# Performance work log

Measured on AMD Instinct MI355X. Metric: run time of the kernel, lower is better.

## Reference

```python
import jax, jax.numpy as jnp
import numpy as np

DIM = 192
WH, WW = 8, 8
N = WH * WW
NUM_HEADS = 6
HEAD_DIM = DIM // NUM_HEADS
SCALE = HEAD_DIM ** (-0.5)
B_ = 4096


def _relative_position_index(Wh, Ww):
    coords = np.stack(np.meshgrid(np.arange(Wh), np.arange(Ww), indexing='ij'))  # [2, Wh, Ww]
    cf = coords.reshape(2, -1)                              # [2, N]
    rel = cf[:, :, None] - cf[:, None, :]                   # [2, N, N]
    rel = rel.transpose(1, 2, 0).astype(np.int64)           # [N, N, 2]
    rel[..., 0] += Wh - 1
    rel[..., 1] += Ww - 1
    rel[..., 0] *= 2 * Ww - 1
    return rel.sum(-1)                                      # [N, N]


REL_IDX = jnp.asarray(_relative_position_index(WH, WW))


def setup_inputs() -> dict:
    key = jax.random.key(0)
    ks = jax.random.split(key, 6)
    x = jax.random.normal(ks[0], (B_, N, DIM), dtype=jnp.float32)
    w_qkv = jax.random.normal(ks[1], (3 * DIM, DIM), dtype=jnp.float32) * (DIM ** -0.5)
    b_qkv = jnp.zeros((3 * DIM,), dtype=jnp.float32)
    w_proj = jax.random.normal(ks[2], (DIM, DIM), dtype=jnp.float32) * (DIM ** -0.5)
    b_proj = jnp.zeros((DIM,), dtype=jnp.float32)
    # torch init is zeros; use small noise so the bias path is exercised
    bias_table = jax.random.normal(ks[3], ((2 * WH - 1) * (2 * WW - 1), NUM_HEADS), dtype=jnp.float32) * 0.02
    return {"x": x, "w_qkv": w_qkv, "b_qkv": b_qkv, "w_proj": w_proj,
            "b_proj": b_proj, "bias_table": bias_table}


def reference(x, w_qkv, b_qkv, w_proj, b_proj, bias_table):
    B, n, C = x.shape
    qkv = jnp.einsum('bnc,dc->bnd', x, w_qkv) + b_qkv        # [B, N, 3C]
    qkv = qkv.reshape(B, n, 3, NUM_HEADS, HEAD_DIM)
    q = qkv[:, :, 0].transpose(0, 2, 1, 3) * SCALE            # [B, H, N, hd]
    k = qkv[:, :, 1].transpose(0, 2, 1, 3)
    v = qkv[:, :, 2].transpose(0, 2, 1, 3)
    attn = jnp.einsum('bhnd,bhmd->bhnm', q, k)                # [B, H, N, N]
    bias = bias_table[REL_IDX]                                # [N, N, H]
    attn = attn + bias.transpose(2, 0, 1)[None]               # broadcast over B
    attn = jax.nn.softmax(attn, axis=-1)
    out = jnp.einsum('bhnm,bhmd->bnhd', attn, v).reshape(B, n, C)
    return jnp.einsum('bnc,dc->bnd', out, w_proj) + b_proj
```

## Files before the change

kernel.cpp:

```cpp
#include <hip/hip_runtime.h>

#define TOK 64
#define CDIM 192
#define NH 6
#define HD 32
#define THREADS 384
#define QSCALE 0.17677669529663687f

#define WQ16_OFF 0
#define WP16_OFF 110592
#define BIAS_OFF 147456
#define WS_HALFS (147456 + 24576)
#define WS_BYTES (WS_HALFS * 2)

typedef _Float16 f16x8 __attribute__((ext_vector_type(8)));
typedef _Float16 f16x4 __attribute__((ext_vector_type(4)));
typedef float f32x4 __attribute__((ext_vector_type(4)));

__device__ __forceinline__ f16x8 ld8(const _Float16* p) {
  return *reinterpret_cast<const f16x8*>(p);
}

__device__ __forceinline__ f16x8 cvt8(const float* __restrict__ p) {
  float4 a = *reinterpret_cast<const float4*>(p);
  float4 c = *reinterpret_cast<const float4*>(p + 4);
  f16x8 r;
  r[0] = (_Float16)a.x; r[1] = (_Float16)a.y; r[2] = (_Float16)a.z; r[3] = (_Float16)a.w;
  r[4] = (_Float16)c.x; r[5] = (_Float16)c.y; r[6] = (_Float16)c.z; r[7] = (_Float16)c.w;
  return r;
}

__device__ __forceinline__ f16x4 pack4(float a, float b, float c, float d) {
  f16x4 r;
  r[0] = (_Float16)a; r[1] = (_Float16)b; r[2] = (_Float16)c; r[3] = (_Float16)d;
  return r;
}

__global__ void prep_ws(const float* __restrict__ wq, const float* __restrict__ wp,
                        const float* __restrict__ bt, _Float16* __restrict__ ws) {
  int i = blockIdx.x * 256 + threadIdx.x;
  if (i < 27648) {
    float4 v = reinterpret_cast<const float4*>(wq)[i];
    f16x4 h;
    h[0] = (_Float16)v.x; h[1] = (_Float16)v.y; h[2] = (_Float16)v.z; h[3] = (_Float16)v.w;
    *reinterpret_cast<f16x4*>(ws + WQ16_OFF + (size_t)i * 4) = h;
  } else if (i < 36864) {
    int j = i - 27648;
    float4 v = reinterpret_cast<const float4*>(wp)[j];
    f16x4 h;
    h[0] = (_Float16)v.x; h[1] = (_Float16)v.y; h[2] = (_Float16)v.z; h[3] = (_Float16)v.w;
    *reinterpret_cast<f16x4*>(ws + WP16_OFF + (size_t)j * 4) = h;
  } else if (i < 61440) {
    int j = i - 36864;
    int hit = j >> 10;
    int l = (j >> 4) & 63;
    int s = j & 15;
    int h = hit >> 2, it = hit & 3;
    int ii = it * 16 + (l & 15);
    int jj = (s >> 2) * 16 + (l >> 4) * 4 + (s & 3);
    int rel = ((ii >> 3) - (jj >> 3) + 7) * 15 + ((ii & 7) - (jj & 7) + 7);
    ws[BIAS_OFF + j] = (_Float16)bt[rel * NH + h];
  }
}

template <bool WS>
__global__ __launch_bounds__(THREADS, 4) void winattn(
    const float* __restrict__ x, const float* __restrict__ w_qkv,
    const float* __restrict__ b_qkv, const float* __restrict__ w_proj,
    const float* __restrict__ b_proj, const float* __restrict__ bias_table,
    const _Float16* __restrict__ ws, float* __restrict__ out) {
  __shared__ __align__(16) _Float16 R1[12288];

  const int tid = threadIdx.x;
  const int h   = tid >> 6;
  const int l   = tid & 63;
  const int l15 = l & 15;
  const int lg  = l >> 4;
  const int b   = blockIdx.x;
  const int sA0 = l15 ^ lg;
  const int sA1 = sA0 ^ 4;
  const f32x4 vzero = {0.f, 0.f, 0.f, 0.f};

  const float* xg = x + (size_t)b * (TOK * CDIM);
#pragma unroll
  for (int kk = 0; kk < 4; ++kk) {
    int q = tid + kk * THREADS;
    int n = q / 24;
    int p = q - n * 24;
    const float* src = xg + q * 8;
    float4 v0 = *reinterpret_cast<const float4*>(src);
    float4 v1 = *reinterpret_cast<const float4*>(src + 4);
    f16x8 h8;
    h8[0] = (_Float16)v0.x; h8[1] = (_Float16)v0.y;
    h8[2] = (_Float16)v0.z; h8[3] = (_Float16)v0.w;
    h8[4] = (_Float16)v1.x; h8[5] = (_Float16)v1.y;
    h8[6] = (_Float16)v1.z; h8[7] = (_Float16)v1.w;
    *reinterpret_cast<f16x8*>(&R1[(p * TOK + (n ^ (p & 7))) * 8]) = h8;
  }
  __syncthreads();

  const _Float16* bxb0 = &R1[(lg * TOK + sA0) * 8];
  const _Float16* bxb1 = &R1[(lg * TOK + sA1) * 8];

  f32x4 aq[2][4], ak[2][4];
#pragma unroll
  for (int mt = 0; mt < 2; ++mt)
#pragma unroll
    for (int nt = 0; nt < 4; ++nt) { aq[mt][nt] = vzero; ak[mt][nt] = vzero; }
  {
    const _Float16* pq0;
    const _Float16* pq1;
    const _Float16* pk0;
    const _Float16* pk1;
    const float* fq0; const float* fq1; const float* fk0; const float* fk1;
    if constexpr (WS) {
      pq0 = ws + WQ16_OFF + (size_t)(h * HD + l15) * CDIM + lg * 8;
      pq1 = pq0 + (size_t)16 * CDIM;
      pk0 = pq0 + (size_t)CDIM * CDIM;
      pk1 = pk0 + (size_t)16 * CDIM;
    } else {
      fq0 = w_qkv + (size_t)(h * HD + l15) * CDIM + lg * 8;
      fq1 = fq0 + (size_t)16 * CDIM;
      fk0 = fq0 + (size_t)CDIM * CDIM;
      fk1 = fk0 + (size_t)16 * CDIM;
    }
#pragma unroll
    for (int ks = 0; ks < 6; ++ks) {
      const _Float16* bb = (ks & 1) ? bxb1 : bxb0;
      f16x8 bx[4];
#pragma unroll
      for (int nt = 0; nt < 4; ++nt)
        bx[nt] = ld8(bb + ks * 2048 + nt * 128);
      f16x8 wqa[2], wka[2];
      if constexpr (WS) {
        wqa[0] = ld8(pq0 + ks * 32); wqa[1] = ld8(pq1 + ks * 32);
        wka[0] = ld8(pk0 + ks * 32); wka[1] = ld8(pk1 + ks * 32);
      } else {
        wqa[0] = cvt8(fq0 + ks * 32); wqa[1] = cvt8(fq1 + ks * 32);
        wka[0] = cvt8(fk0 + ks * 32); wka[1] = cvt8(fk1 + ks * 32);
      }
      __builtin_amdgcn_s_setprio(1);
#pragma unroll
      for (int mt = 0; mt < 2; ++mt)
#pragma unroll
        for (int nt = 0; nt < 4; ++nt) {
          aq[mt][nt] = __builtin_amdgcn_mfma_f32_16x16x32_f16(wqa[mt], bx[nt], aq[mt][nt], 0, 0, 0);
          ak[mt][nt] = __builtin_amdgcn_mfma_f32_16x16x32_f16(wka[mt], bx[nt], ak[mt][nt], 0, 0, 0);
        }
      __builtin_amdgcn_s_setprio(0);
    }
  }
  f16x4 qp[2][4], kp[2][4];
#pragma unroll
  for (int mt = 0; mt < 2; ++mt) {
    float4 bq = *reinterpret_cast<const float4*>(b_qkv + h * HD + mt * 16 + lg * 4);
    float4 bk = *reinterpret_cast<const float4*>(b_qkv + CDIM + h * HD + mt * 16 + lg * 4);
#pragma unroll
    for (int nt = 0; nt < 4; ++nt) {
      qp[mt][nt] = pack4((aq[mt][nt][0] + bq.x) * QSCALE, (aq[mt][nt][1] + bq.y) * QSCALE,
                         (aq[mt][nt][2] + bq.z) * QSCALE, (aq[mt][nt][3] + bq.w) * QSCALE);
      kp[mt][nt] = pack4(ak[mt][nt][0] + bk.x, ak[mt][nt][1] + bk.y,
                         ak[mt][nt][2] + bk.z, ak[mt][nt][3] + bk.w);
    }
  }

  f16x4 vp[4][2];
  {
    f32x4 av[4][2];
#pragma unroll
    for (int mt = 0; mt < 4; ++mt)
#pragma unroll
      for (int ct = 0; ct < 2; ++ct) av[mt][ct] = vzero;
    const _Float16* pv0;
    const _Float16* pv1;
    const float* fv0; const float* fv1;
    if constexpr (WS) {
      pv0 = ws + WQ16_OFF + (size_t)(2 * CDIM + h * HD + l15) * CDIM + lg * 8;
      pv1 = pv0 + (size_t)16 * CDIM;
    } else {
      fv0 = w_qkv + (size_t)(2 * CDIM + h * HD + l15) * CDIM + lg * 8;
      fv1 = fv0 + (size_t)16 * CDIM;
    }
#pragma unroll
    for (int ks = 0; ks < 6; ++ks) {
      const _Float16* bb = (ks & 1) ? bxb1 : bxb0;
      f16x8 a[4];
#pragma unroll
      for (int mt = 0; mt < 4; ++mt)
        a[mt] = ld8(bb + ks * 2048 + mt * 128);
      f16x8 bw[2];
      if constexpr (WS) { bw[0] = ld8(pv0 + ks * 32); bw[1] = ld8(pv1 + ks * 32); }
      else              { bw[0] = cvt8(fv0 + ks * 32); bw[1] = cvt8(fv1 + ks * 32); }
      __builtin_amdgcn_s_setprio(1);
#pragma unroll
      for (int mt = 0; mt < 4; ++mt)
#pragma unroll
        for (int ct = 0; ct < 2; ++ct)
          av[mt][ct] = __builtin_amdgcn_mfma_f32_16x16x32_f16(a[mt], bw[ct], av[mt][ct], 0, 0, 0);
      __builtin_amdgcn_s_setprio(0);
    }
    float bv0 = b_qkv[2 * CDIM + h * HD + l15];
    float bv1 = b_qkv[2 * CDIM + h * HD + 16 + l15];
#pragma unroll
    for (int s = 0; s < 4; ++s) {
      vp[s][0] = pack4(av[s][0][0] + bv0, av[s][0][1] + bv0, av[s][0][2] + bv0, av[s][0][3] + bv0);
      vp[s][1] = pack4(av[s][1][0] + bv1, av[s][1][1] + bv1, av[s][1][2] + bv1, av[s][1][3] + bv1);
    }
  }
  __syncthreads();

#pragma unroll
  for (int it = 0; it < 4; ++it) {
    f32x4 st[4];
    __builtin_amdgcn_s_setprio(1);
#pragma unroll
    for (int jt = 0; jt < 4; ++jt) {
      st[jt] = __builtin_amdgcn_mfma_f32_16x16x16f16(kp[0][jt], qp[0][it], vzero, 0, 0, 0);
      st[jt] = __builtin_amdgcn_mfma_f32_16x16x16f16(kp[1][jt], qp[1][it], st[jt], 0, 0, 0);
    }
    __builtin_amdgcn_s_setprio(0);
    if constexpr (WS) {
      const _Float16* bw = ws + BIAS_OFF + ((h * 4 + it) * 64 + l) * 16;
      f16x8 b0 = ld8(bw), b1 = ld8(bw + 8);
#pragma unroll
      for (int jt = 0; jt < 4; ++jt)
#pragma unroll
        for (int r = 0; r < 4; ++r)
          st[jt][r] += (float)((jt < 2) ? b0[jt * 4 + r] : b1[(jt - 2) * 4 + r]);
    } else {
      int i = it * 16 + l15, yi = i >> 3, xi = i & 7;
#pragma unroll
      for (int jt = 0; jt < 4; ++jt)
#pragma unroll
        for (int r = 0; r < 4; ++r) {
          int j = jt * 16 + lg * 4 + r, yj = j >> 3, xj = j & 7;
          st[jt][r] += bias_table[(((yi - yj + 7) * 15 + (xi - xj + 7)) * NH + h)];
        }
    }
    float m = st[0][0];
#pragma unroll
    for (int jt = 0; jt < 4; ++jt)
#pragma unroll
      for (int r = 0; r < 4; ++r) m = fmaxf(m, st[jt][r]);
    m = fmaxf(m, __shfl_xor(m, 16, 64));
    m = fmaxf(m, __shfl_xor(m, 32, 64));
    float sum = 0.f;
#pragma unroll
    for (int jt = 0; jt < 4; ++jt)
#pragma unroll
      for (int r = 0; r < 4; ++r) { st[jt][r] = __expf(st[jt][r] - m); sum += st[jt][r]; }
    sum += __shfl_xor(sum, 16, 64);
    sum += __shfl_xor(sum, 32, 64);
    float inv = 1.f / sum;
    f32x4 o[2] = {vzero, vzero};
#pragma unroll
    for (int s = 0; s < 4; ++s) {
      f16x4 pp = pack4(st[s][0] * inv, st[s][1] * inv, st[s][2] * inv, st[s][3] * inv);
      __builtin_amdgcn_s_setprio(1);
      o[0] = __builtin_amdgcn_mfma_f32_16x16x16f16(pp, vp[s][0], o[0], 0, 0, 0);
      o[1] = __builtin_amdgcn_mfma_f32_16x16x16f16(pp, vp[s][1], o[1], 0, 0, 0);
      __builtin_amdgcn_s_setprio(0);
    }
#pragma unroll
    for (int ct = 0; ct < 2; ++ct) {
      int c = h * HD + ct * 16 + l15;
      int op = c >> 3, s7 = op & 7;
      int lgx = lg ^ (s7 >> 2);
      int base = (op * TOK + it * 16 + lgx * 4) * 8 + (c & 7);
#pragma unroll
      for (int r = 0; r < 4; ++r)
        R1[base + (r ^ (s7 & 3)) * 8] = (_Float16)o[ct][r];
    }
  }
  __syncthreads();

  {
    const int e0 = h * 16 + l15;
    const int e1 = e0 + 96;
    f32x4 pa0[4], pa1[4];
#pragma unroll
    for (int mt = 0; mt < 4; ++mt) { pa0[mt] = vzero; pa1[mt] = vzero; }
    const _Float16* pw0;
    const _Float16* pw1;
    const float* fw0; const float* fw1;
    if constexpr (WS) {
      pw0 = ws + WP16_OFF + (size_t)e0 * CDIM + lg * 8;
      pw1 = pw0 + (size_t)96 * CDIM;
    } else {
      fw0 = w_proj + (size_t)e0 * CDIM + lg * 8;
      fw1 = fw0 + (size_t)96 * CDIM;
    }
#pragma unroll
    for (int ks = 0; ks < 6; ++ks) {
      const _Float16* bb = (ks & 1) ? bxb1 : bxb0;
      f16x8 a[4];
#pragma unroll
      for (int mt = 0; mt < 4; ++mt)
        a[mt] = ld8(bb + ks * 2048 + mt * 128);
      f16x8 w0, w1;
      if constexpr (WS) { w0 = ld8(pw0 + ks * 32); w1 = ld8(pw1 + ks * 32); }
      else              { w0 = cvt8(fw0 + ks * 32); w1 = cvt8(fw1 + ks * 32); }
      __builtin_amdgcn_s_setprio(1);
#pragma unroll
      for (int mt = 0; mt < 4; ++mt) {
        pa0[mt] = __builtin_amdgcn_mfma_f32_16x16x32_f16(a[mt], w0, pa0[mt], 0, 0, 0);
        pa1[mt] = __builtin_amdgcn_mfma_f32_16x16x32_f16(a[mt], w1, pa1[mt], 0, 0, 0);
      }
      __builtin_amdgcn_s_setprio(0);
    }
    float bp0 = b_proj[e0], bp1 = b_proj[e1];
#pragma unroll
    for (int mt = 0; mt < 4; ++mt) {
#pragma unroll
      for (int r = 0; r < 4; ++r) {
        int n = mt * 16 + lg * 4 + r;
        out[((size_t)b * TOK + n) * CDIM + e0] = pa0[mt][r] + bp0;
        out[((size_t)b * TOK + n) * CDIM + e1] = pa1[mt][r] + bp1;
      }
    }
  }
}

extern "C" void kernel_launch(void* const* d_in, const int* in_sizes, int n_in,
                              void* d_out, int out_size, void* d_ws, size_t ws_size,
                              hipStream_t stream) {
  const float* x          = (const float*)d_in[0];
  const float* w_qkv      = (const float*)d_in[1];
  const float* b_qkv      = (const float*)d_in[2];
  const float* w_proj     = (const float*)d_in[3];
  const float* b_proj     = (const float*)d_in[4];
  const float* bias_table = (const float*)d_in[5];
  float* out = (float*)d_out;
  int B = in_sizes[0] / (TOK * CDIM);

  if (ws_size >= (size_t)WS_BYTES) {
    _Float16* ws = (_Float16*)d_ws;
    hipLaunchKernelGGL(prep_ws, dim3(240), dim3(256), 0, stream,
                       w_qkv, w_proj, bias_table, ws);
    hipLaunchKernelGGL(winattn<true>, dim3(B), dim3(THREADS), 0, stream,
                       x, w_qkv, b_qkv, w_proj, b_proj, bias_table, ws, out);
  } else {
    hipLaunchKernelGGL(winattn<false>, dim3(B), dim3(THREADS), 0, stream,
                       x, w_qkv, b_qkv, w_proj, b_proj, bias_table,
                       (const _Float16*)nullptr, out);
  }
}
```

Measured before the change: 242.8 us.

## Make window attention persistent with double-buffered x prefetch

Converts the one-block-per-window kernel into a persistent kernel capped at 512 blocks. Each block loops over windows and prefetches the next window's x into registers during the output projection, then stores it into a second LDS buffer. The projection MFMA operands are swapped so each lane writes float4 rows of output instead of scalar stores. This costs double the LDS (48KB per block), which may limit occupancy, and leaves fewer blocks in flight to hide latency.

```diff
diff --git a/kernel.cpp b/kernel.cpp
--- a/kernel.cpp
+++ b/kernel.cpp
@@ -5,6 +5,7 @@
 #define NH 6
 #define HD 32
 #define THREADS 384
+#define GRID_MAX 512
 #define QSCALE 0.17677669529663687f
 
 #define WQ16_OFF 0
@@ -24,6 +25,13 @@
 __device__ __forceinline__ f16x8 cvt8(const float* __restrict__ p) {
   float4 a = *reinterpret_cast<const float4*>(p);
   float4 c = *reinterpret_cast<const float4*>(p + 4);
+  f16x8 r;
+  r[0] = (_Float16)a.x; r[1] = (_Float16)a.y; r[2] = (_Float16)a.z; r[3] = (_Float16)a.w;
+  r[4] = (_Float16)c.x; r[5] = (_Float16)c.y; r[6] = (_Float16)c.z; r[7] = (_Float16)c.w;
+  return r;
+}
+
+__device__ __forceinline__ f16x8 cvt2(float4 a, float4 c) {
   f16x8 r;
   r[0] = (_Float16)a.x; r[1] = (_Float16)a.y; r[2] = (_Float16)a.z; r[3] = (_Float16)a.w;
   r[4] = (_Float16)c.x; r[5] = (_Float16)c.y; r[6] = (_Float16)c.z; r[7] = (_Float16)c.w;
@@ -68,62 +76,79 @@
     const float* __restrict__ x, const float* __restrict__ w_qkv,
     const float* __restrict__ b_qkv, const float* __restrict__ w_proj,
     const float* __restrict__ b_proj, const float* __restrict__ bias_table,
-    const _Float16* __restrict__ ws, float* __restrict__ out) {
-  __shared__ __align__(16) _Float16 R1[12288];
+    const _Float16* __restrict__ ws, float* __restrict__ out, int B) {
+  __shared__ __align__(16) _Float16 X[2][12288];
 
   const int tid = threadIdx.x;
   const int h   = tid >> 6;
   const int l   = tid & 63;
   const int l15 = l & 15;
   const int lg  = l >> 4;
-  const int b   = blockIdx.x;
   const int sA0 = l15 ^ lg;
   const int sA1 = sA0 ^ 4;
+  const int G   = gridDim.x;
   const f32x4 vzero = {0.f, 0.f, 0.f, 0.f};
 
-  const float* xg = x + (size_t)b * (TOK * CDIM);
+  int goff[4], soff[4];
 #pragma unroll
   for (int kk = 0; kk < 4; ++kk) {
     int q = tid + kk * THREADS;
     int n = q / 24;
-    int p = q - n * 24;
-    const float* src = xg + q * 8;
-    float4 v0 = *reinterpret_cast<const float4*>(src);
-    float4 v1 = *reinterpret_cast<const float4*>(src + 4);
-    f16x8 h8;
-    h8[0] = (_Float16)v0.x; h8[1] = (_Float16)v0.y;
-    h8[2] = (_Float16)v0.z; h8[3] = (_Float16)v0.w;
-    h8[4] = (_Float16)v1.x; h8[5] = (_Float16)v1.y;
-    h8[6] = (_Float16)v1.z; h8[7] = (_Float16)v1.w;
-    *reinterpret_cast<f16x8*>(&R1[(p * TOK + (n ^ (p & 7))) * 8]) = h8;
+    int pp = q - n * 24;
+    goff[kk] = q * 8;
+    soff[kk] = (pp * TOK + (n ^ (pp & 7))) * 8;
+  }
+
+  const _Float16 *pq0 = nullptr, *pq1 = nullptr, *pk0 = nullptr, *pk1 = nullptr,
+                 *pv0 = nullptr, *pv1 = nullptr, *pw0 = nullptr, *pw1 = nullptr;
+  const float *fq0 = nullptr, *fq1 = nullptr, *fk0 = nullptr, *fk1 = nullptr,
+              *fv0 = nullptr, *fv1 = nullptr, *fw0 = nullptr, *fw1 = nullptr;
+  if constexpr (WS) {
+    pq0 = ws + WQ16_OFF + (size_t)(h * HD + l15) * CDIM + lg * 8;
+    pq1 = pq0 + (size_t)16 * CDIM;
+    pk0 = pq0 + (size_t)CDIM * CDIM;
+    pk1 = pk0 + (size_t)16 * CDIM;
+    pv0 = pq0 + (size_t)2 * CDIM * CDIM;
+    pv1 = pv0 + (size_t)16 * CDIM;
+    pw0 = ws + WP16_OFF + (size_t)(h * 16 + l15) * CDIM + lg * 8;
+    pw1 = pw0 + (size_t)96 * CDIM;
+  } else {
+    fq0 = w_qkv + (size_t)(h * HD + l15) * CDIM + lg * 8;
+    fq1 = fq0 + (size_t)16 * CDIM;
+    fk0 = fq0 + (size_t)CDIM * CDIM;
+    fk1 = fk0 + (size_t)16 * CDIM;
+    fv0 = fq0 + (size_t)2 * CDIM * CDIM;
+    fv1 = fv0 + (size_t)16 * CDIM;
+    fw0 = w_proj + (size_t)(h * 16 + l15) * CDIM + lg * 8;
+    fw1 = fw0 + (size_t)96 * CDIM;
+  }
+
+  {
+    const float* xg = x + (size_t)blockIdx.x * (TOK * CDIM);
+#pragma unroll
+    for (int kk = 0; kk < 4; ++kk) {
+      float4 v0 = *reinterpret_cast<const float4*>(xg + goff[kk]);
+      float4 v1 = *reinterpret_cast<const float4*>(xg + goff[kk] + 4);
+      *reinterpret_cast<f16x8*>(&X[0][soff[kk]]) = cvt2(v0, v1);
+    }
   }
   __syncthreads();
 
-  const _Float16* bxb0 = &R1[(lg * TOK + sA0) * 8];
-  const _Float16* bxb1 = &R1[(lg * TOK + sA1) * 8];
-
-  f32x4 aq[2][4], ak[2][4];
-#pragma unroll
-  for (int mt = 0; mt < 2; ++mt)
-#pragma unroll
-    for (int nt = 0; nt < 4; ++nt) { aq[mt][nt] = vzero; ak[mt][nt] = vzero; }
-  {
-    const _Float16* pq0;
-    const _Float16* pq1;
-    const _Float16* pk0;
-    const _Float16* pk1;
-    const float* fq0; const float* fq1; const float* fk0; const float* fk1;
-    if constexpr (WS) {
-      pq0 = ws + WQ16_OFF + (size_t)(h * HD + l15) * CDIM + lg * 8;
-      pq1 = pq0 + (size_t)16 * CDIM;
-      pk0 = pq0 + (size_t)CDIM * CDIM;
-      pk1 = pk0 + (size_t)16 * CDIM;
-    } else {
-      fq0 = w_qkv + (size_t)(h * HD + l15) * CDIM + lg * 8;
-      fq1 = fq0 + (size_t)16 * CDIM;
-      fk0 = fq0 + (size_t)CDIM * CDIM;
-      fk1 = fk0 + (size_t)16 * CDIM;
-    }
+  int p = 0;
+  const int NW = (B + G - 1) / G;
+#pragma unroll 1
+  for (int wi = 0; wi < NW; ++wi) {
+    const int win = blockIdx.x + wi * G;
+    if (win >= B) break;
+    _Float16* Xa = X[p];
+    const _Float16* bxb0 = &Xa[(lg * TOK + sA0) * 8];
+    const _Float16* bxb1 = &Xa[(lg * TOK + sA1) * 8];
+
+    f32x4 aq[2][4], ak[2][4];
+#pragma unroll
+    for (int mt = 0; mt < 2; ++mt)
+#pragma unroll
+      for (int nt = 0; nt < 4; ++nt) { aq[mt][nt] = vzero; ak[mt][nt] = vzero; }
 #pragma unroll
     for (int ks = 0; ks < 6; ++ks) {
       const _Float16* bb = (ks & 1) ? bxb1 : bxb0;
@@ -149,175 +174,181 @@
         }
       __builtin_amdgcn_s_setprio(0);
     }
-  }
-  f16x4 qp[2][4], kp[2][4];
-#pragma unroll
-  for (int mt = 0; mt < 2; ++mt) {
-    float4 bq = *reinterpret_cast<const float4*>(b_qkv + h * HD + mt * 16 + lg * 4);
-    float4 bk = *reinterpret_cast<const float4*>(b_qkv + CDIM + h * HD + mt * 16 + lg * 4);
-#pragma unroll
-    for (int nt = 0; nt < 4; ++nt) {
-      qp[mt][nt] = pack4((aq[mt][nt][0] + bq.x) * QSCALE, (aq[mt][nt][1] + bq.y) * QSCALE,
-                         (aq[mt][nt][2] + bq.z) * QSCALE, (aq[mt][nt][3] + bq.w) * QSCALE);
-      kp[mt][nt] = pack4(ak[mt][nt][0] + bk.x, ak[mt][nt][1] + bk.y,
-                         ak[mt][nt][2] + bk.z, ak[mt][nt][3] + bk.w);
-    }
-  }
-
-  f16x4 vp[4][2];
-  {
-    f32x4 av[4][2];
-#pragma unroll
-    for (int mt = 0; mt < 4; ++mt)
-#pragma unroll
-      for (int ct = 0; ct < 2; ++ct) av[mt][ct] = vzero;
-    const _Float16* pv0;
-    const _Float16* pv1;
-    const float* fv0; const float* fv1;
-    if constexpr (WS) {
-      pv0 = ws + WQ16_OFF + (size_t)(2 * CDIM + h * HD + l15) * CDIM + lg * 8;
-      pv1 = pv0 + (size_t)16 * CDIM;
-    } else {
-      fv0 = w_qkv + (size_t)(2 * CDIM + h * HD + l15) * CDIM + lg * 8;
-      fv1 = fv0 + (size_t)16 * CDIM;
-    }
-#pragma unroll
-    for (int ks = 0; ks < 6; ++ks) {
-      const _Float16* bb = (ks & 1) ? bxb1 : bxb0;
-      f16x8 a[4];
+    f16x4 qp[2][4], kp[2][4];
+#pragma unroll
+    for (int mt = 0; mt < 2; ++mt) {
+      float4 bq = *reinterpret_cast<const float4*>(b_qkv + h * HD + mt * 16 + lg * 4);
+      float4 bk = *reinterpret_cast<const float4*>(b_qkv + CDIM + h * HD + mt * 16 + lg * 4);
+#pragma unroll
+      for (int nt = 0; nt < 4; ++nt) {
+        qp[mt][nt] = pack4((aq[mt][nt][0] + bq.x) * QSCALE, (aq[mt][nt][1] + bq.y) * QSCALE,
+                           (aq[mt][nt][2] + bq.z) * QSCALE, (aq[mt][nt][3] + bq.w) * QSCALE);
+        kp[mt][nt] = pack4(ak[mt][nt][0] + bk.x, ak[mt][nt][1] + bk.y,
+                           ak[mt][nt][2] + bk.z, ak[mt][nt][3] + bk.w);
+      }
+    }
+
+    f16x4 vp[4][2];
+    {
+      f32x4 av[4][2];
 #pragma unroll
       for (int mt = 0; mt < 4; ++mt)
-        a[mt] = ld8(bb + ks * 2048 + mt * 128);
-      f16x8 bw[2];
-      if constexpr (WS) { bw[0] = ld8(pv0 + ks * 32); bw[1] = ld8(pv1 + ks * 32); }
-      else              { bw[0] = cvt8(fv0 + ks * 32); bw[1] = cvt8(fv1 + ks * 32); }
+#pragma unroll
+        for (int ct = 0; ct < 2; ++ct) av[mt][ct] = vzero;
+#pragma unroll
+      for (int ks = 0; ks < 6; ++ks) {
+        const _Float16* bb = (ks & 1) ? bxb1 : bxb0;
+        f16x8 a[4];
+#pragma unroll
+        for (int mt = 0; mt < 4; ++mt)
+          a[mt] = ld8(bb + ks * 2048 + mt * 128);
+        f16x8 bw[2];
+        if constexpr (WS) { bw[0] = ld8(pv0 + ks * 32); bw[1] = ld8(pv1 + ks * 32); }
+        else              { bw[0] = cvt8(fv0 + ks * 32); bw[1] = cvt8(fv1 + ks * 32); }
+        __builtin_amdgcn_s_setprio(1);
+#pragma unroll
+        for (int mt = 0; mt < 4; ++mt)
+#pragma unroll
+          for (int ct = 0; ct < 2; ++ct)
+            av[mt][ct] = __builtin_amdgcn_mfma_f32_16x16x32_f16(a[mt], bw[ct], av[mt][ct], 0, 0, 0);
+        __builtin_amdgcn_s_setprio(0);
+      }
+      float bv0 = b_qkv[2 * CDIM + h * HD + l15];
+      float bv1 = b_qkv[2 * CDIM + h * HD + 16 + l15];
+#pragma unroll
+      for (int s = 0; s < 4; ++s) {
+        vp[s][0] = pack4(av[s][0][0] + bv0, av[s][0][1] + bv0, av[s][0][2] + bv0, av[s][0][3] + bv0);
+        vp[s][1] = pack4(av[s][1][0] + bv1, av[s][1][1] + bv1, av[s][1][2] + bv1, av[s][1][3] + bv1);
+      }
+    }
+    __syncthreads();
+
+#pragma unroll
+    for (int it = 0; it < 4; ++it) {
+      f32x4 st[4];
       __builtin_amdgcn_s_setprio(1);
 #pragma unroll
-      for (int mt = 0; mt < 4; ++mt)
-#pragma unroll
-        for (int ct = 0; ct < 2; ++ct)
-          av[mt][ct] = __builtin_amdgcn_mfma_f32_16x16x32_f16(a[mt], bw[ct], av[mt][ct], 0, 0, 0);
+      for (int jt = 0; jt < 4; ++jt) {
+        st[jt] = __builtin_amdgcn_mfma_f32_16x16x16f16(kp[0][jt], qp[0][it], vzero, 0, 0, 0);
+        st[jt] = __builtin_amdgcn_mfma_f32_16x16x16f16(kp[1][jt], qp[1][it], st[jt], 0, 0, 0);
+      }
       __builtin_amdgcn_s_setprio(0);
-    }
-    float bv0 = b_qkv[2 * CDIM + h * HD + l15];
-    float bv1 = b_qkv[2 * CDIM + h * HD + 16 + l15];
-#pragma unroll
-    for (int s = 0; s < 4; ++s) {
-      vp[s][0] = pack4(av[s][0][0] + bv0, av[s][0][1] + bv0, av[s][0][2] + bv0, av[s][0][3] + bv0);
-      vp[s][1] = pack4(av[s][1][0] + bv1, av[s][1][1] + bv1, av[s][1][2] + bv1, av[s][1][3] + bv1);
-    }
-  }
-  __syncthreads();
-
-#pragma unroll
-  for (int it = 0; it < 4; ++it) {
-    f32x4 st[4];
-    __builtin_amdgcn_s_setprio(1);
-#pragma unroll
-    for (int jt = 0; jt < 4; ++jt) {
-      st[jt] = __builtin_amdgcn_mfma_f32_16x16x16f16(kp[0][jt], qp[0][it], vzero, 0, 0, 0);
-      st[jt] = __builtin_amdgcn_mfma_f32_16x16x16f16(kp[1][jt], qp[1][it], st[jt], 0, 0, 0);
-    }
-    __builtin_amdgcn_s_setprio(0);
-    if constexpr (WS) {
-      const _Float16* bw = ws + BIAS_OFF + ((h * 4 + it) * 64 + l) * 16;
-      f16x8 b0 = ld8(bw), b1 = ld8(bw + 8);
+      if constexpr (WS) {
+        const _Float16* bw = ws + BIAS_OFF + ((h * 4 + it) * 64 + l) * 16;
+        f16x8 b0 = ld8(bw), b1 = ld8(bw + 8);
+#pragma unroll
+        for (int jt = 0; jt < 4; ++jt)
+#pragma unroll
+          for (int r = 0; r < 4; ++r)
+            st[jt][r] += (float)((jt < 2) ? b0[jt * 4 + r] : b1[(jt - 2) * 4 + r]);
+      } else {
+        int i = it * 16 + l15, yi = i >> 3, xi = i & 7;
+#pragma unroll
+        for (int jt = 0; jt < 4; ++jt)
+#pragma unroll
+          for (int r = 0; r < 4; ++r) {
+            int j = jt * 16 + lg * 4 + r, yj = j >> 3, xj = j & 7;
+            st[jt][r] += bias_table[(((yi - yj + 7) * 15 + (xi - xj + 7)) * NH + h)];
+          }
+      }
+      float m = st[0][0];
 #pragma unroll
       for (int jt = 0; jt < 4; ++jt)
 #pragma unroll
+        for (int r = 0; r < 4; ++r) m = fmaxf(m, st[jt][r]);
+      m = fmaxf(m, __shfl_xor(m, 16, 64));
+      m = fmaxf(m, __shfl_xor(m, 32, 64));
+      float sum = 0.f;
+#pragma unroll
+      for (int jt = 0; jt < 4; ++jt)
+#pragma unroll
+        for (int r = 0; r < 4; ++r) { st[jt][r] = __expf(st[jt][r] - m); sum += st[jt][r]; }
+      sum += __shfl_xor(sum, 16, 64);
+      sum += __shfl_xor(sum, 32, 64);
+      float inv = 1.f / sum;
+      f32x4 o[2] = {vzero, vzero};
+#pragma unroll
+      for (int s = 0; s < 4; ++s) {
+        f16x4 pp2 = pack4(st[s][0] * inv, st[s][1] * inv, st[s][2] * inv, st[s][3] * inv);
+        __builtin_amdgcn_s_setprio(1);
+        o[0] = __builtin_amdgcn_mfma_f32_16x16x16f16(pp2, vp[s][0], o[0], 0, 0, 0);
+        o[1] = __builtin_amdgcn_mfma_f32_16x16x16f16(pp2, vp[s][1], o[1], 0, 0, 0);
+        __builtin_amdgcn_s_setprio(0);
+      }
+#pragma unroll
+      for (int ct = 0; ct < 2; ++ct) {
+        int c = h * HD + ct * 16 + l15;
+        int op = c >> 3, s7 = op & 7;
+        int lgx = lg ^ (s7 >> 2);
+        int base = (op * TOK + it * 16 + lgx * 4) * 8 + (c & 7);
+#pragma unroll
         for (int r = 0; r < 4; ++r)
-          st[jt][r] += (float)((jt < 2) ? b0[jt * 4 + r] : b1[(jt - 2) * 4 + r]);
-    } else {
-      int i = it * 16 + l15, yi = i >> 3, xi = i & 7;
-#pragma unroll
-      for (int jt = 0; jt < 4; ++jt)
-#pragma unroll
-        for (int r = 0; r < 4; ++r) {
-          int j = jt * 16 + lg * 4 + r, yj = j >> 3, xj = j & 7;
-          st[jt][r] += bias_table[(((yi - yj + 7) * 15 + (xi - xj + 7)) * NH + h)];
+          Xa[base + (r ^ (s7 & 3)) * 8] = (_Float16)o[ct][r];
+      }
+    }
+    __syncthreads();
+
+    const int win2 = win + G;
+    float4 pf0a, pf0b, pf1a, pf1b, pf2a, pf2b, pf3a, pf3b;
+    if (win2 < B) {
+      const float* xg2 = x + (size_t)win2 * (TOK * CDIM);
+      pf0a = *reinterpret_cast<const float4*>(xg2 + goff[0]);
+      pf0b = *reinterpret_cast<const float4*>(xg2 + goff[0] + 4);
+      pf1a = *reinterpret_cast<const float4*>(xg2 + goff[1]);
+      pf1b = *reinterpret_cast<const float4*>(xg2 + goff[1] + 4);
+      pf2a = *reinterpret_cast<const float4*>(xg2 + goff[2]);
+      pf2b = *reinterpret_cast<const float4*>(xg2 + goff[2] + 4);
+      pf3a = *reinterpret_cast<const float4*>(xg2 + goff[3]);
+      pf3b = *reinterpret_cast<const float4*>(xg2 + goff[3] + 4);
+    }
+
+    {
+      f32x4 pa0[4], pa1[4];
+#pragma unroll
+      for (int nt = 0; nt < 4; ++nt) { pa0[nt] = vzero; pa1[nt] = vzero; }
+#pragma unroll
+      for (int ks = 0; ks < 6; ++ks) {
+        const _Float16* bb = (ks & 1) ? bxb1 : bxb0;
+        f16x8 a[4];
+#pragma unroll
+        for (int nt = 0; nt < 4; ++nt)
+          a[nt] = ld8(bb + ks * 2048 + nt * 128);
+        f16x8 w0, w1;
+        if constexpr (WS) { w0 = ld8(pw0 + ks * 32); w1 = ld8(pw1 + ks * 32); }
+        else              { w0 = cvt8(fw0 + ks * 32); w1 = cvt8(fw1 + ks * 32); }
+        __builtin_amdgcn_s_setprio(1);
+#pragma unroll
+        for (int nt = 0; nt < 4; ++nt) {
+          pa0[nt] = __builtin_amdgcn_mfma_f32_16x16x32_f16(w0, a[nt], pa0[nt], 0, 0, 0);
+          pa1[nt] = __builtin_amdgcn_mfma_f32_16x16x32_f16(w1, a[nt], pa1[nt], 0, 0, 0);
         }
-    }
-    float m = st[0][0];
-#pragma unroll
-    for (int jt = 0; jt < 4; ++jt)
-#pragma unroll
-      for (int r = 0; r < 4; ++r) m = fmaxf(m, st[jt][r]);
-    m = fmaxf(m, __shfl_xor(m, 16, 64));
-    m = fmaxf(m, __shfl_xor(m, 32, 64));
-    float sum = 0.f;
-#pragma unroll
-    for (int jt = 0; jt < 4; ++jt)
-#pragma unroll
-      for (int r = 0; r < 4; ++r) { st[jt][r] = __expf(st[jt][r] - m); sum += st[jt][r]; }
-    sum += __shfl_xor(sum, 16, 64);
-    sum += __shfl_xor(sum, 32, 64);
-    float inv = 1.f / sum;
-    f32x4 o[2] = {vzero, vzero};
-#pragma unroll
-    for (int s = 0; s < 4; ++s) {
-      f16x4 pp = pack4(st[s][0] * inv, st[s][1] * inv, st[s][2] * inv, st[s][3] * inv);
-      __builtin_amdgcn_s_setprio(1);
-      o[0] = __builtin_amdgcn_mfma_f32_16x16x16f16(pp, vp[s][0], o[0], 0, 0, 0);
-      o[1] = __builtin_amdgcn_mfma_f32_16x16x16f16(pp, vp[s][1], o[1], 0, 0, 0);
-      __builtin_amdgcn_s_setprio(0);
-    }
-#pragma unroll
-    for (int ct = 0; ct < 2; ++ct) {
-      int c = h * HD + ct * 16 + l15;
-      int op = c >> 3, s7 = op & 7;
-      int lgx = lg ^ (s7 >> 2);
-      int base = (op * TOK + it * 16 + lgx * 4) * 8 + (c & 7);
-#pragma unroll
-      for (int r = 0; r < 4; ++r)
-        R1[base + (r ^ (s7 & 3)) * 8] = (_Float16)o[ct][r];
-    }
-  }
-  __syncthreads();
-
-  {
-    const int e0 = h * 16 + l15;
-    const int e1 = e0 + 96;
-    f32x4 pa0[4], pa1[4];
-#pragma unroll
-    for (int mt = 0; mt < 4; ++mt) { pa0[mt] = vzero; pa1[mt] = vzero; }
-    const _Float16* pw0;
-    const _Float16* pw1;
-    const float* fw0; const float* fw1;
-    if constexpr (WS) {
-      pw0 = ws + WP16_OFF + (size_t)e0 * CDIM + lg * 8;
-      pw1 = pw0 + (size_t)96 * CDIM;
-    } else {
-      fw0 = w_proj + (size_t)e0 * CDIM + lg * 8;
-      fw1 = fw0 + (size_t)96 * CDIM;
-    }
-#pragma unroll
-    for (int ks = 0; ks < 6; ++ks) {
-      const _Float16* bb = (ks & 1) ? bxb1 : bxb0;
-      f16x8 a[4];
-#pragma unroll
-      for (int mt = 0; mt < 4; ++mt)
-        a[mt] = ld8(bb + ks * 2048 + mt * 128);
-      f16x8 w0, w1;
-      if constexpr (WS) { w0 = ld8(pw0 + ks * 32); w1 = ld8(pw1 + ks * 32); }
-      else              { w0 = cvt8(fw0 + ks * 32); w1 = cvt8(fw1 + ks * 32); }
-      __builtin_amdgcn_s_setprio(1);
-#pragma unroll
-      for (int mt = 0; mt < 4; ++mt) {
-        pa0[mt] = __builtin_amdgcn_mfma_f32_16x16x32_f16(a[mt], w0, pa0[mt], 0, 0, 0);
-        pa1[mt] = __builtin_amdgcn_mfma_f32_16x16x32_f16(a[mt], w1, pa1[mt], 0, 0, 0);
-      }
-      __builtin_amdgcn_s_setprio(0);
-    }
-    float bp0 = b_proj[e0], bp1 = b_proj[e1];
-#pragma unroll
-    for (int mt = 0; mt < 4; ++mt) {
-#pragma unroll
-      for (int r = 0; r < 4; ++r) {
-        int n = mt * 16 + lg * 4 + r;
-        out[((size_t)b * TOK + n) * CDIM + e0] = pa0[mt][r] + bp0;
-        out[((size_t)b * TOK + n) * CDIM + e1] = pa1[mt][r] + bp1;
-      }
-    }
+        __builtin_amdgcn_s_setprio(0);
+      }
+      float* outw = out + (size_t)win * (TOK * CDIM);
+      float4 bp0 = *reinterpret_cast<const float4*>(b_proj + h * 16 + lg * 4);
+      float4 bp1 = *reinterpret_cast<const float4*>(b_proj + h * 16 + 96 + lg * 4);
+#pragma unroll
+      for (int nt = 0; nt < 4; ++nt) {
+        float4 r0, r1;
+        r0.x = pa0[nt][0] + bp0.x; r0.y = pa0[nt][1] + bp0.y;
+        r0.z = pa0[nt][2] + bp0.z; r0.w = pa0[nt][3] + bp0.w;
+        r1.x = pa1[nt][0] + bp1.x; r1.y = pa1[nt][1] + bp1.y;
+        r1.z = pa1[nt][2] + bp1.z; r1.w = pa1[nt][3] + bp1.w;
+        float* rowp = outw + (nt * 16 + l15) * CDIM + h * 16 + lg * 4;
+        *reinterpret_cast<float4*>(rowp) = r0;
+        *reinterpret_cast<float4*>(rowp + 96) = r1;
+      }
+    }
+
+    if (win2 < B) {
+      _Float16* Xn = X[p ^ 1];
+      *reinterpret_cast<f16x8*>(&Xn[soff[0]]) = cvt2(pf0a, pf0b);
+      *reinterpret_cast<f16x8*>(&Xn[soff[1]]) = cvt2(pf1a, pf1b);
+      *reinterpret_cast<f16x8*>(&Xn[soff[2]]) = cvt2(pf2a, pf2b);
+      *reinterpret_cast<f16x8*>(&Xn[soff[3]]) = cvt2(pf3a, pf3b);
+    }
+    __syncthreads();
+    p ^= 1;
   }
 }
 
@@ -332,16 +363,17 @@
   const float* bias_table = (const float*)d_in[5];
   float* out = (float*)d_out;
   int B = in_sizes[0] / (TOK * CDIM);
+  int G = B < GRID_MAX ? B : GRID_MAX;
 
   if (ws_size >= (size_t)WS_BYTES) {
     _Float16* ws = (_Float16*)d_ws;
     hipLaunchKernelGGL(prep_ws, dim3(240), dim3(256), 0, stream,
                        w_qkv, w_proj, bias_table, ws);
-    hipLaunchKernelGGL(winattn<true>, dim3(B), dim3(THREADS), 0, stream,
-                       x, w_qkv, b_qkv, w_proj, b_proj, bias_table, ws, out);
+    hipLaunchKernelGGL(winattn<true>, dim3(G), dim3(THREADS), 0, stream,
+                       x, w_qkv, b_qkv, w_proj, b_proj, bias_table, ws, out, B);
   } else {
-    hipLaunchKernelGGL(winattn<false>, dim3(B), dim3(THREADS), 0, stream,
+    hipLaunchKernelGGL(winattn<false>, dim3(G), dim3(THREADS), 0, stream,
                        x, w_qkv, b_qkv, w_proj, b_proj, bias_table,
-                       (const _Float16*)nullptr, out);
-  }
-}
+                       (const _Float16*)nullptr, out, B);
+  }
+}
```

Result: slower. 474.8 us (+95.6%).
